# Kernel optimization log

Hardware: AMD Instinct MI355X
Metric: run time of the kernel (lower is better)

## Reference

```python
import jax, jax.numpy as jnp
import numpy as np

S = 4   # stride
NH = 4  # n_heads
NP = 4  # n_points


def conv2d(x, w, b, pad):
    out = jax.lax.conv_general_dilated(x, w, (1, 1), [(pad, pad), (pad, pad)],
                                       dimension_numbers=('NCHW', 'OIHW', 'NCHW'))
    return out + b[None, :, None, None]


def leaky(x):
    return jnp.where(x >= 0, x, 0.1 * x)


def seq_net(x, w0, b0, w1, b1, w2, b2, w3, b3):
    x = leaky(conv2d(x, w0, b0, 0))
    x = leaky(conv2d(x, w1, b1, 1))
    x = leaky(conv2d(x, w2, b2, 1))
    return conv2d(x, w3, b3, 0)


def fold_s(x, C, hs, ws):
    # inverse of unfold(kernel=S, stride=S): (N, C*S*S, hs*ws) -> (N, C, hs*S, ws*S)
    N = x.shape[0]
    x = x.reshape(N, C, S, S, hs, ws)
    return x.transpose(0, 1, 4, 2, 5, 3).reshape(N, C, hs * S, ws * S)


def unfold_s(x):
    # (N, C, h, w) -> (N, C*S*S, h//S, w//S), kernel=S, stride=S
    N, C, h, w = x.shape
    hs, ws = h // S, w // S
    x = x.reshape(N, C, hs, S, ws, S).transpose(0, 1, 3, 5, 2, 4)
    return x.reshape(N, C * S * S, hs, ws)


def avgpool_s(x):
    # adaptive_avg_pool2d (h,w)->(h/S,w/S) == mean over SxS blocks
    N, C, h, w = x.shape
    return x.reshape(N, C, h // S, S, w // S, S).mean(axis=(3, 5))


def grid_sample_nearest(img, grid):
    # img (N,C,H,W); grid (N,A,B,2) normalized; nearest, zeros padding, align_corners=True
    N, C, H, W = img.shape
    ix = jnp.round((grid[..., 0] + 1.0) * 0.5 * (W - 1))
    iy = jnp.round((grid[..., 1] + 1.0) * 0.5 * (H - 1))
    valid = (ix >= 0) & (ix <= W - 1) & (iy >= 0) & (iy <= H - 1)
    ixi = jnp.clip(ix, 0, W - 1).astype(jnp.int32)
    iyi = jnp.clip(iy, 0, H - 1).astype(jnp.int32)
    out = jax.vmap(lambda im, yy, xx: im[:, yy, xx])(img, iyi, ixi)  # (N,C,A,B)
    return out * valid[:, None].astype(img.dtype)


def ltff_forward(anchor_feat, sparse_feat_set_s1, flow_buffers,
                 so_w0, so_b0, so_w1, so_b1, so_w2, so_b2, so_w3, so_b3,
                 aw_w0, aw_b0, aw_w1, aw_b1, aw_w2, aw_b2, aw_w3, aw_b3,
                 fusion_w, fusion_b):
    n, c, h, w = anchor_feat.shape
    t = sparse_feat_set_s1.shape[1]
    hs, ws = h // S, w // S
    ch = c // NH  # per-head channels

    gy, gx = jnp.meshgrid(jnp.arange(hs), jnp.arange(ws), indexing='ij')
    loc_ref = jnp.stack([gx, gy], 0).astype(flow_buffers.dtype)[None, None]  # (1,1,2,hs,ws)
    location_feat = flow_buffers + loc_ref  # (n,t,2,hs,ws)

    # flow-warp the (strided) sparse feature set; align_corners=True norm uses dim-1
    gf = location_feat.transpose(0, 1, 3, 4, 2)  # (n,t,hs,ws,2)
    gfx = 2.0 * gf[..., 0] / max(ws - 1, 1) - 1.0
    gfy = 2.0 * gf[..., 1] / max(hs - 1, 1) - 1.0
    grid1 = jnp.stack([gfx, gfy], -1).reshape(n * t, hs, ws, 2)

    sp = sparse_feat_set_s1.reshape(n * t, c * S * S, hs, ws)
    warp = grid_sample_nearest(sp, grid1)
    out_res = fold_s(warp.reshape(n * t, c * S * S, hs * ws), c, hs, ws)  # (n*t,c,h,w)
    out_ori = fold_s(sp.reshape(n * t, c * S * S, hs * ws), c, hs, ws)

    extra = jnp.concatenate([avgpool_s(out_ori), avgpool_s(out_res),
                             flow_buffers.reshape(n * t, 2, hs, ws)], axis=1)  # (n*t,2c+2,hs,ws)

    offsets = seq_net(extra, so_w0, so_b0, so_w1, so_b1, so_w2, so_b2, so_w3, so_b3)
    offsets = offsets.reshape(n * t, NH * NP, 2, hs, ws)
    attn = seq_net(extra, aw_w0, aw_b0, aw_w1, aw_b1, aw_w2, aw_b2, aw_w3, aw_b3)
    attn = (attn.reshape(n, t, NH, NP, hs, ws)
                .transpose(0, 2, 4, 5, 1, 3)
                .reshape(n * NH, hs, ws, t * NP))
    attn = jax.nn.softmax(attn, axis=-1)

    og = location_feat.reshape(n * t, 1, 2, hs, ws) + offsets  # (n*t, NH*NP, 2, hs, ws)
    og = og.transpose(0, 1, 3, 4, 2)
    ogx = 2.0 * og[..., 0] / ws - 1.0  # original divides by dim (not dim-1) here
    ogy = 2.0 * og[..., 1] / hs - 1.0
    og = jnp.stack([ogx, ogy], -1).reshape(n, t, NH, NP, hs * ws, 2)
    og = og.transpose(0, 1, 2, 4, 3, 5).reshape(n * t * NH, hs * ws, NP, 2)

    vals = out_ori.reshape(n * t * NH, ch, h, w)
    vals = unfold_s(vals)  # (n*t*NH, ch*S*S, hs, ws)
    sampled = grid_sample_nearest(vals, og)  # (n*t*NH, ch*S*S, hs*ws, NP)
    sampled = (sampled.reshape(n, t, NH, ch * S * S, hs, ws, NP)
                      .transpose(0, 2, 3, 4, 5, 1, 6)
                      .reshape(n * NH, ch * S * S, hs, ws, t * NP))

    out = (sampled * attn[:, None]).sum(-1)  # (n*NH, ch*S*S, hs, ws)
    out = fold_s(out.reshape(n * NH, ch * S * S, hs * ws), ch, hs, ws).reshape(n, c, h, w)
    out = conv2d(out, fusion_w, fusion_b, 1) + anchor_feat
    return out


def setup_inputs():
    key = jax.random.key(0)
    ks = jax.random.split(key, 16)
    n, t, c, h, w = 2, 3, 128, 192, 192
    hs, ws = h // S, w // S
    cin = 2 * c + 2  # 258
    m = 64
    f32 = jnp.float32
    def rn(k, shape, scale=1.0):
        return jax.random.normal(k, shape, dtype=f32) * scale
    return {
        'curr_feat': rn(ks[0], (n, c, h, w)),
        'anchor_feat': rn(ks[1], (n, c, h, w)),
        'sparse_feat_set_s1': rn(ks[2], (n, t, c * S * S, hs, ws)),
        'flow_buffers': rn(ks[3], (n, t, 2, hs, ws)),
        'so_w0': rn(ks[4], (m, cin, 1, 1), 0.05), 'so_b0': jnp.zeros((m,), f32),
        'so_w1': rn(ks[5], (m, m, 3, 3), 0.05), 'so_b1': jnp.zeros((m,), f32),
        'so_w2': rn(ks[6], (m, m, 3, 3), 0.05), 'so_b2': jnp.zeros((m,), f32),
        'so_w3': rn(ks[7], (NH * NP * 2, m, 1, 1), 0.05), 'so_b3': jnp.zeros((NH * NP * 2,), f32),
        'aw_w0': rn(ks[8], (m, cin, 1, 1), 0.05), 'aw_b0': jnp.zeros((m,), f32),
        'aw_w1': rn(ks[9], (m, m, 3, 3), 0.05), 'aw_b1': jnp.zeros((m,), f32),
        'aw_w2': rn(ks[10], (m, m, 3, 3), 0.05), 'aw_b2': jnp.zeros((m,), f32),
        'aw_w3': rn(ks[11], (NH * NP, m, 1, 1), 0.05), 'aw_b3': jnp.zeros((NH * NP,), f32),
        'fusion_w': rn(ks[12], (c, c, 3, 3), 0.02), 'fusion_b': jnp.zeros((c,), f32),
    }


def reference(curr_feat, anchor_feat, sparse_feat_set_s1, flow_buffers,
              so_w0, so_b0, so_w1, so_b1, so_w2, so_b2, so_w3, so_b3,
              aw_w0, aw_b0, aw_w1, aw_b1, aw_w2, aw_b2, aw_w3, aw_b3,
              fusion_w, fusion_b):
    # curr_feat is accepted by the original forward but never used
    return ltff_forward(anchor_feat, sparse_feat_set_s1, flow_buffers,
                        so_w0, so_b0, so_w1, so_b1, so_w2, so_b2, so_w3, so_b3,
                        aw_w0, aw_b0, aw_w1, aw_b1, aw_w2, aw_b2, aw_w3, aw_b3,
                        fusion_w, fusion_b)
```

## Files before the change

kernel.cpp:

```cpp
#include <hip/hip_runtime.h>

typedef unsigned short u16;
typedef unsigned int u32;
typedef __attribute__((ext_vector_type(8))) short bf16x8;
typedef __attribute__((ext_vector_type(4))) float f32x4;

#define HS   48
#define WSB  48
#define NPIX 2304
#define CCH  128
#define NT   6
#define CIN  258
#define HH   192
#define WW   192

#define EXTRA_OFF  0ull
#define OUTIMG_OFF 0ull
#define XA_OFF     4718592ull
#define XB_OFF     6488064ull
#define OFFS_OFF   8257536ull
#define ARAW_OFF   8699904ull
#define WT_OFF     8921088ull
#define SPT_OFF    4718592ull
#define ATTNW_OFF  11796480ull
#define SIDX_OFF   12017664ull
#define WBF_OFF    12238848ull

static __device__ __forceinline__ float leaky_f(float v) { return v >= 0.f ? v : 0.1f * v; }
static __device__ __forceinline__ u16 f2bf(float f) {
    u32 u = __float_as_uint(f);
    u = (u + 0x7fffu + ((u >> 16) & 1u)) >> 16;
    return (u16)u;
}
static __device__ __forceinline__ float bf2f(u16 v) {
    u32 u = ((u32)v) << 16;
    return __uint_as_float(u);
}

__global__ __launch_bounds__(256) void k_wprep(const float* __restrict__ fw, u16* __restrict__ wbf) {
    int i = blockIdx.x * 256 + threadIdx.x;
    int j  = i & 7;
    int g  = (i >> 3) & 3;
    int oc = (i >> 5) & 127;
    int kcd = i >> 12;
    int d = kcd >> 2, kc = kcd & 3;
    int ic = kc * 32 + g * 8 + j;
    wbf[i] = f2bf(fw[((size_t)oc * 128 + ic) * 9 + d]);
}

__global__ __launch_bounds__(256) void k_wprep2(const float* __restrict__ so_w1, const float* __restrict__ aw_w1,
                                                const float* __restrict__ so_w2, const float* __restrict__ aw_w2,
                                                float* __restrict__ wT) {
    int i = blockIdx.x * 256 + threadIdx.x;
    int l   = i / 73728;
    int r1  = i % 73728;
    int net = r1 / 36864;
    int r   = r1 % 36864;
    int ic  = r / 576;
    int t2  = r % 576;
    int tap = t2 >> 6, oc = t2 & 63;
    const float* src = l ? (net ? aw_w2 : so_w2) : (net ? aw_w1 : so_w1);
    wT[i] = src[(size_t)oc * 576 + ic * 9 + tap];
}

__global__ __launch_bounds__(256) void k_avgpool(const float* __restrict__ sp,
                                                 float* __restrict__ extra) {
    int idx = blockIdx.x * 256 + threadIdx.x;
    if (idx >= NT * CCH * NPIX) return;
    int pix = idx % NPIX;
    int cc  = (idx / NPIX) % CCH;
    int nt  = idx / (NPIX * CCH);
    const float* p = sp + ((size_t)nt * 2048 + (size_t)cc * 16) * NPIX + pix;
    float s = 0.f;
#pragma unroll
    for (int k = 0; k < 16; k++) s += p[(size_t)k * NPIX];
    extra[((size_t)nt * CIN + cc) * NPIX + pix] = s * 0.0625f;
}

__global__ __launch_bounds__(256) void k_extra_rest(const float* __restrict__ flow,
                                                    float* __restrict__ extra) {
    int idx = blockIdx.x * 256 + threadIdx.x;
    if (idx >= NT * 130 * NPIX) return;
    int pix = idx % NPIX;
    int cc  = (idx / NPIX) % 130;
    int nt  = idx / (NPIX * 130);
    float fx = flow[((size_t)nt * 2 + 0) * NPIX + pix];
    float fy = flow[((size_t)nt * 2 + 1) * NPIX + pix];
    if (cc >= 128) {
        extra[((size_t)nt * CIN + 256 + (cc - 128)) * NPIX + pix] = (cc == 128) ? fx : fy;
        return;
    }
    int x = pix % WSB, y = pix / WSB;
    float locx = fx + (float)x;
    float locy = fy + (float)y;
    float gfx = 2.0f * locx / 47.0f - 1.0f;
    float gfy = 2.0f * locy / 47.0f - 1.0f;
    float rx = rintf(((gfx + 1.0f) * 0.5f) * 47.0f);
    float ry = rintf(((gfy + 1.0f) * 0.5f) * 47.0f);
    bool valid = (rx >= 0.f) && (rx <= 47.f) && (ry >= 0.f) && (ry <= 47.f);
    int sx = (int)fminf(fmaxf(rx, 0.f), 47.f);
    int sy = (int)fminf(fmaxf(ry, 0.f), 47.f);
    float v = valid ? extra[((size_t)nt * CIN + cc) * NPIX + sy * WSB + sx] : 0.f;
    extra[((size_t)nt * CIN + 128 + cc) * NPIX + pix] = v;
}

__global__ __launch_bounds__(256) void k_conv1x1_l0(const float* __restrict__ extra,
                                                    const float* __restrict__ w_so, const float* __restrict__ b_so,
                                                    const float* __restrict__ w_aw, const float* __restrict__ b_aw,
                                                    float* __restrict__ xa) {
    __shared__ float ws_[16 * CIN];
    int tile = blockIdx.x;
    int nt   = blockIdx.y;
    int z    = blockIdx.z;
    int net = z >> 2, ocg = z & 3;
    const float* wsel = net ? w_aw : w_so;
    const float* bsel = net ? b_aw : b_so;
    for (int i = threadIdx.x; i < 16 * CIN; i += 256)
        ws_[i] = wsel[(size_t)(ocg * 16) * CIN + i];
    __syncthreads();
    int pix = tile * 256 + threadIdx.x;
    float acc[16];
#pragma unroll
    for (int o = 0; o < 16; o++) acc[o] = bsel[ocg * 16 + o];
    const float* in = extra + (size_t)nt * CIN * NPIX + pix;
    for (int ci = 0; ci < CIN; ci++) {
        float v = in[(size_t)ci * NPIX];
#pragma unroll
        for (int o = 0; o < 16; o++) acc[o] = fmaf(ws_[o * CIN + ci], v, acc[o]);
    }
    float* op = xa + (((size_t)net * NT + nt) * 64 + ocg * 16) * NPIX + pix;
#pragma unroll
    for (int o = 0; o < 16; o++) op[(size_t)o * NPIX] = leaky_f(acc[o]);
}

__global__ __launch_bounds__(256) void k_conv3x3(const float* __restrict__ xin,
                                                 const float* __restrict__ wT,
                                                 const float* __restrict__ b_so, const float* __restrict__ b_aw,
                                                 float* __restrict__ xout) {
    __shared__ float At[16][6][24];
    __shared__ float Bt[16][9][64];
    int tid = threadIdx.x;
    int txq = tid & 3, tyq = (tid >> 2) & 3, ocg = tid >> 4;
    int st = blockIdx.x;
    int x0 = (st % 3) * 16, y0 = (st / 3) * 4;
    int nt = blockIdx.y, net = blockIdx.z;
    const float* in  = xin + ((size_t)net * NT + nt) * 64 * NPIX;
    const float* wTn = wT + (size_t)net * 36864;
    const float* bsel = net ? b_aw : b_so;

    float acc[4][4];
#pragma unroll
    for (int o = 0; o < 4; o++) {
        float bv = bsel[ocg * 4 + o];
#pragma unroll
        for (int p = 0; p < 4; p++) acc[o][p] = bv;
    }

    for (int c0 = 0; c0 < 64; c0 += 16) {
        __syncthreads();
        for (int i = tid; i < 1728; i += 256) {
            int ic = i / 108, r = i % 108;
            int ry = r / 18, rx = r % 18;
            int gy = y0 + ry - 1, gx = x0 + rx - 1;
            float v = 0.f;
            if (gy >= 0 && gy < HS && gx >= 0 && gx < WSB)
                v = in[(size_t)(c0 + ic) * NPIX + gy * WSB + gx];
            At[ic][ry][rx] = v;
        }
        {
            const float* src = wTn + (size_t)c0 * 576;
            float* dst = &Bt[0][0][0];
            for (int i = tid; i < 9216; i += 256) dst[i] = src[i];
        }
        __syncthreads();
#pragma unroll 2
        for (int ic = 0; ic < 16; ic++) {
#pragma unroll
            for (int dy = 0; dy < 3; dy++) {
                f32x4 a0 = *reinterpret_cast<const f32x4*>(&At[ic][tyq + dy][4 * txq]);
                f32x4 a1 = *reinterpret_cast<const f32x4*>(&At[ic][tyq + dy][4 * txq + 4]);
#pragma unroll
                for (int dx = 0; dx < 3; dx++) {
                    f32x4 bv = *reinterpret_cast<const f32x4*>(&Bt[ic][dy * 3 + dx][4 * ocg]);
#pragma unroll
                    for (int p = 0; p < 4; p++) {
                        float av = (dx + p < 4) ? a0[dx + p] : a1[dx + p - 4];
#pragma unroll
                        for (int o = 0; o < 4; o++)
                            acc[o][p] = fmaf(bv[o], av, acc[o][p]);
                    }
                }
            }
        }
    }

    int py = y0 + tyq, pxb = x0 + 4 * txq;
#pragma unroll
    for (int o = 0; o < 4; o++) {
        f32x4 res;
#pragma unroll
        for (int p = 0; p < 4; p++) res[p] = leaky_f(acc[o][p]);
        float* op = xout + (((size_t)net * NT + nt) * 64 + ocg * 4 + o) * NPIX + py * WSB + pxb;
        *reinterpret_cast<f32x4*>(op) = res;
    }
}

__global__ __launch_bounds__(256) void k_conv1x1_l3(const float* __restrict__ xin,
                                                    const float* __restrict__ w_so, const float* __restrict__ b_so,
                                                    const float* __restrict__ w_aw, const float* __restrict__ b_aw,
                                                    float* __restrict__ offs, float* __restrict__ araw) {
    int pix = blockIdx.x * 256 + threadIdx.x;
    int nt = blockIdx.y;
    int net = blockIdx.z;
    const float* in = xin + ((size_t)net * NT + nt) * 64 * NPIX + pix;
    if (net == 0) {
        float acc[32];
#pragma unroll
        for (int o = 0; o < 32; o++) acc[o] = b_so[o];
        for (int ci = 0; ci < 64; ci++) {
            float v = in[(size_t)ci * NPIX];
#pragma unroll
            for (int o = 0; o < 32; o++) acc[o] = fmaf(w_so[o * 64 + ci], v, acc[o]);
        }
#pragma unroll
        for (int o = 0; o < 32; o++) offs[((size_t)nt * 32 + o) * NPIX + pix] = acc[o];
    } else {
        float acc[16];
#pragma unroll
        for (int o = 0; o < 16; o++) acc[o] = b_aw[o];
        for (int ci = 0; ci < 64; ci++) {
            float v = in[(size_t)ci * NPIX];
#pragma unroll
            for (int o = 0; o < 16; o++) acc[o] = fmaf(w_aw[o * 64 + ci], v, acc[o]);
        }
#pragma unroll
        for (int o = 0; o < 16; o++) araw[((size_t)nt * 16 + o) * NPIX + pix] = acc[o];
    }
}

__global__ __launch_bounds__(256) void k_softmax_idx(const float* __restrict__ araw,
                                                     const float* __restrict__ offs,
                                                     const float* __restrict__ flow,
                                                     float* __restrict__ attnw, int* __restrict__ sidx) {
    int idx = blockIdx.x * 256 + threadIdx.x;
    if (idx >= 2 * 4 * NPIX) return;
    int pix  = idx % NPIX;
    int head = (idx / NPIX) & 3;
    int n    = idx / (NPIX * 4);
    int x = pix % WSB, y = pix / WSB;
    float a[12];
#pragma unroll
    for (int t = 0; t < 3; t++)
#pragma unroll
        for (int p = 0; p < 4; p++)
            a[t * 4 + p] = araw[(((size_t)(n * 3 + t)) * 16 + head * 4 + p) * NPIX + pix];
    float mx = a[0];
#pragma unroll
    for (int k = 1; k < 12; k++) mx = fmaxf(mx, a[k]);
    float ssum = 0.f;
#pragma unroll
    for (int k = 0; k < 12; k++) { a[k] = expf(a[k] - mx); ssum += a[k]; }
    float inv = 1.0f / ssum;
#pragma unroll
    for (int t = 0; t < 3; t++) {
        int nt = n * 3 + t;
        float fx = flow[((size_t)nt * 2 + 0) * NPIX + pix];
        float fy = flow[((size_t)nt * 2 + 1) * NPIX + pix];
        float locx = fx + (float)x;
        float locy = fy + (float)y;
#pragma unroll
        for (int p = 0; p < 4; p++) {
            int hp = head * 4 + p;
            float gx_ = locx + offs[(((size_t)nt) * 32 + hp * 2 + 0) * NPIX + pix];
            float gy_ = locy + offs[(((size_t)nt) * 32 + hp * 2 + 1) * NPIX + pix];
            float ngx = 2.0f * gx_ / 48.0f - 1.0f;
            float ngy = 2.0f * gy_ / 48.0f - 1.0f;
            float rx = rintf(((ngx + 1.0f) * 0.5f) * 47.0f);
            float ry = rintf(((ngy + 1.0f) * 0.5f) * 47.0f);
            bool valid = (rx >= 0.f) && (rx <= 47.f) && (ry >= 0.f) && (ry <= 47.f);
            int sx = (int)fminf(fmaxf(rx, 0.f), 47.f);
            int sy = (int)fminf(fmaxf(ry, 0.f), 47.f);
            int k = t * 4 + p;
            attnw[(size_t)idx * 12 + k] = valid ? a[k] * inv : 0.f;
            sidx[(size_t)idx * 12 + k]  = sy * WSB + sx;
        }
    }
}

__global__ __launch_bounds__(256) void k_transpose(const float* __restrict__ sp,
                                                   u16* __restrict__ spT, int n) {
    __shared__ float tile[64][65];
    int tid = threadIdx.x;
    int pix0 = blockIdx.x * 64;
    int ch0  = blockIdx.y * 64;
    int tl   = blockIdx.z;
    int nt = n * 3 + tl;
    const float* base = sp + ((size_t)nt * 2048 + ch0) * NPIX + pix0;
#pragma unroll
    for (int k = 0; k < 16; k++) {
        int row = k * 4 + (tid >> 6);
        int col = tid & 63;
        tile[row][col] = base[(size_t)row * NPIX + col];
    }
    __syncthreads();
#pragma unroll
    for (int k = 0; k < 2; k++) {
        int task = k * 256 + tid;
        int pl = task >> 3;
        int c0 = (task & 7) * 8;
        u16 pk[8];
#pragma unroll
        for (int j = 0; j < 8; j++) pk[j] = f2bf(tile[c0 + j][pl]);
        *reinterpret_cast<int4*>(spT + ((size_t)tl * NPIX + pix0 + pl) * 2048 + ch0 + c0) =
            *reinterpret_cast<const int4*>(pk);
    }
}

__global__ __launch_bounds__(256) void k_gather2(const u16* __restrict__ spT,
                                                 const float* __restrict__ attnw,
                                                 const int* __restrict__ sidx,
                                                 u16* __restrict__ outimg, int n) {
    __shared__ u16 sArr[2048 + 128];
    int tid = threadIdx.x;
    int pix = blockIdx.x;
    int y = pix / WSB, x = pix % WSB;
    int h = tid >> 6;
    int lane = tid & 63;
    size_t ab = ((size_t)(n * 4 + h) * NPIX + pix) * 12;
    float acc[8] = {};
#pragma unroll
    for (int t = 0; t < 3; t++) {
#pragma unroll
        for (int p = 0; p < 4; p++) {
            int k = t * 4 + p;
            float w = attnw[ab + k];
            int idx = sidx[ab + k];
            bf16x8 v = *reinterpret_cast<const bf16x8*>(
                spT + ((size_t)t * NPIX + idx) * 2048 + h * 512 + lane * 8);
#pragma unroll
            for (int j = 0; j < 8; j++)
                acc[j] = fmaf(w, bf2f((u16)v[j]), acc[j]);
        }
    }
    int c0 = h * 512 + lane * 8;
    int si = c0 + (c0 >> 4);
    u16 pk[8];
#pragma unroll
    for (int j = 0; j < 8; j++) pk[j] = f2bf(acc[j]);
    *reinterpret_cast<int4*>(&sArr[si]) = *reinterpret_cast<const int4*>(pk);
    __syncthreads();
    int opix = tid >> 4;
    int oc0 = (tid & 15) * 8;
    u16 ov[8];
#pragma unroll
    for (int j = 0; j < 8; j++) {
        int oc = oc0 + j;
        int ch = (oc >> 5) * 512 + (oc & 31) * 16 + opix;
        ov[j] = sArr[ch + (ch >> 4)];
    }
    int hq = y * 4 + (opix >> 2);
    int wq = x * 4 + (opix & 3);
    *reinterpret_cast<int4*>(outimg + (((size_t)(n * HH + hq) * WW + wq) << 7) + oc0) =
        *reinterpret_cast<const int4*>(ov);
}

__global__ __launch_bounds__(256, 3) void k_fusion_mfma(const u16* __restrict__ img,
                                                        const u16* __restrict__ wbf,
                                                        const float* __restrict__ bias,
                                                        const float* __restrict__ anchor,
                                                        float* __restrict__ out) {
    __shared__ __align__(16) u16 lds_in[180 * 128];

    const int tid = threadIdx.x;
    const int px0 = blockIdx.x * 16;
    const int py0 = blockIdx.y * 8;
    const int nb  = blockIdx.z >> 1;
    const int ocq = blockIdx.z & 1;
    const int lane = tid & 63;
    const int w = tid >> 6;
    const int r = lane & 15, g = lane >> 4;

    char* lin_b = reinterpret_cast<char*>(lds_in);

    for (int i = tid; i < 180 * 16; i += 256) {
        int p = i >> 4, c16 = i & 15;
        int hy = p / 18, hx = p % 18;
        int gy = py0 + hy - 1, gx = px0 + hx - 1;
        int4 v = make_int4(0, 0, 0, 0);
        if (gy >= 0 && gy < HH && gx >= 0 && gx < WW)
            v = *reinterpret_cast<const int4*>(img + (((size_t)(nb * HH + gy) * WW + gx) << 7) + (c16 << 3));
        *reinterpret_cast<int4*>(lin_b + p * 256 + (((c16 ^ (p & 7)) << 4))) = v;
    }

    const u16* wb = wbf + (size_t)(ocq * 64 + r) * 32 + g * 8;

    f32x4 acc[2][4] = {};
    bf16x8 b[2][4];
#pragma unroll
    for (int n = 0; n < 4; n++)
        b[0][n] = *reinterpret_cast<const bf16x8*>(wb + (size_t)n * 512);

    __syncthreads();

#pragma unroll
    for (int ph = 0; ph < 36; ph++) {
        const int d = ph >> 2, kc = ph & 3;
        const int dy = d / 3, dx = d % 3;
        if (ph < 35) {
#pragma unroll
            for (int n = 0; n < 4; n++)
                b[(ph + 1) & 1][n] = *reinterpret_cast<const bf16x8*>(
                    wb + (size_t)(ph + 1) * 4096 + (size_t)n * 512);
        }
        const int c16 = kc * 4 + g;
        bf16x8 a[2];
#pragma unroll
        for (int m = 0; m < 2; m++) {
            int hp = (2 * w + m + dy) * 18 + (r + dx);
            a[m] = *reinterpret_cast<const bf16x8*>(lin_b + hp * 256 + (((c16 ^ (hp & 7)) << 4)));
        }
#pragma unroll
        for (int m = 0; m < 2; m++)
#pragma unroll
            for (int n = 0; n < 4; n++)
                acc[m][n] = __builtin_amdgcn_mfma_f32_16x16x32_bf16(a[m], b[ph & 1][n], acc[m][n], 0, 0, 0);
    }

    float bs[4];
#pragma unroll
    for (int n = 0; n < 4; n++) bs[n] = bias[ocq * 64 + n * 16 + r];
#pragma unroll
    for (int m = 0; m < 2; m++) {
        int gy = py0 + 2 * w + m;
#pragma unroll
        for (int n = 0; n < 4; n++) {
            int oc = ocq * 64 + n * 16 + r;
            size_t oa = ((size_t)(nb * CCH + oc)) * (HH * WW) + (size_t)gy * WW + px0 + g * 4;
            f32x4 av = *reinterpret_cast<const f32x4*>(anchor + oa);
            f32x4 res;
#pragma unroll
            for (int q = 0; q < 4; q++) res[q] = acc[m][n][q] + bs[n] + av[q];
            *reinterpret_cast<f32x4*>(out + oa) = res;
        }
    }
}

extern "C" void kernel_launch(void* const* d_in, const int* in_sizes, int n_in,
                              void* d_out, int out_size, void* d_ws, size_t ws_size,
                              hipStream_t stream) {
    (void)in_sizes; (void)n_in; (void)out_size; (void)ws_size;
    const float* anchor = (const float*)d_in[1];
    const float* sp     = (const float*)d_in[2];
    const float* flow   = (const float*)d_in[3];
    const float* so_w0 = (const float*)d_in[4];  const float* so_b0 = (const float*)d_in[5];
    const float* so_w1 = (const float*)d_in[6];  const float* so_b1 = (const float*)d_in[7];
    const float* so_w2 = (const float*)d_in[8];  const float* so_b2 = (const float*)d_in[9];
    const float* so_w3 = (const float*)d_in[10]; const float* so_b3 = (const float*)d_in[11];
    const float* aw_w0 = (const float*)d_in[12]; const float* aw_b0 = (const float*)d_in[13];
    const float* aw_w1 = (const float*)d_in[14]; const float* aw_b1 = (const float*)d_in[15];
    const float* aw_w2 = (const float*)d_in[16]; const float* aw_b2 = (const float*)d_in[17];
    const float* aw_w3 = (const float*)d_in[18]; const float* aw_b3 = (const float*)d_in[19];
    const float* fw    = (const float*)d_in[20]; const float* fb    = (const float*)d_in[21];

    float* ws     = (float*)d_ws;
    float* extra  = ws + EXTRA_OFF;
    float* xa     = ws + XA_OFF;
    float* xb     = ws + XB_OFF;
    float* offs   = ws + OFFS_OFF;
    float* araw   = ws + ARAW_OFF;
    float* wT     = ws + WT_OFF;
    float* attnw  = ws + ATTNW_OFF;
    int*   sidx   = (int*)(ws + SIDX_OFF);
    u16*   wbf    = (u16*)(ws + WBF_OFF);
    u16*   spT    = (u16*)(ws + SPT_OFF);
    u16*   outimg = (u16*)(ws + OUTIMG_OFF);
    float* outp   = (float*)d_out;

    k_wprep<<<dim3(576), 256, 0, stream>>>(fw, wbf);
    k_wprep2<<<dim3(576), 256, 0, stream>>>(so_w1, aw_w1, so_w2, aw_w2, wT);
    k_avgpool<<<dim3((NT * CCH * NPIX + 255) / 256), 256, 0, stream>>>(sp, extra);
    k_extra_rest<<<dim3((NT * 130 * NPIX + 255) / 256), 256, 0, stream>>>(flow, extra);
    k_conv1x1_l0<<<dim3(9, 6, 8), 256, 0, stream>>>(extra, so_w0, so_b0, aw_w0, aw_b0, xa);
    k_conv3x3<<<dim3(36, 6, 2), 256, 0, stream>>>(xa, wT, so_b1, aw_b1, xb);
    k_conv3x3<<<dim3(36, 6, 2), 256, 0, stream>>>(xb, wT + 73728, so_b2, aw_b2, xa);
    k_conv1x1_l3<<<dim3(9, 6, 2), 256, 0, stream>>>(xa, so_w3, so_b3, aw_w3, aw_b3, offs, araw);
    k_softmax_idx<<<dim3((2 * 4 * NPIX + 255) / 256), 256, 0, stream>>>(araw, offs, flow, attnw, sidx);
    for (int n = 0; n < 2; n++) {
        k_transpose<<<dim3(36, 32, 3), 256, 0, stream>>>(sp, spT, n);
        k_gather2<<<dim3(NPIX), 256, 0, stream>>>(spT, attnw, sidx, outimg, n);
    }
    k_fusion_mfma<<<dim3(WW / 16, HH / 8, 4), 256, 0, stream>>>(outimg, wbf, fb, anchor, outp);
}
```

Baseline: 297.0 us.

## Fuse avgpool with bf16 transpose of sparse features into one pass

Adds a kernel that reads each 64x64 tile of the sparse feature set once, writes the bf16 pixel-major transpose for all frames, and computes the 4x4-channel average pooling from the same shared-memory tile. This replaces the separate avgpool pass and the per-batch transpose passes, so the large input is read once instead of twice. It needs a larger workspace layout, and the old path is kept as a fallback when the workspace is too small.

```diff
diff --git a/kernel.cpp b/kernel.cpp
--- a/kernel.cpp
+++ b/kernel.cpp
@@ -25,6 +25,19 @@
 #define ATTNW_OFF  11796480ull
 #define SIDX_OFF   12017664ull
 #define WBF_OFF    12238848ull
+
+#define SPT2_OFF    0ull
+#define EXTRA2_OFF  14155776ull
+#define OUTIMG2_OFF 14155776ull
+#define XA2_OFF     17722368ull
+#define XB2_OFF     19491840ull
+#define OFFS2_OFF   21261312ull
+#define ARAW2_OFF   21703680ull
+#define WT2_OFF     21924864ull
+#define ATTNW2_OFF  22072320ull
+#define SIDX2_OFF   22293504ull
+#define WBF2_OFF    22514688ull
+#define TOTAL2_F32  22588416ull
 
 static __device__ __forceinline__ float leaky_f(float v) { return v >= 0.f ? v : 0.1f * v; }
 static __device__ __forceinline__ u16 f2bf(float f) {
@@ -75,6 +88,44 @@
 #pragma unroll
     for (int k = 0; k < 16; k++) s += p[(size_t)k * NPIX];
     extra[((size_t)nt * CIN + cc) * NPIX + pix] = s * 0.0625f;
+}
+
+__global__ __launch_bounds__(256) void k_spprep(const float* __restrict__ sp,
+                                                u16* __restrict__ spT2,
+                                                float* __restrict__ extra) {
+    __shared__ float tile[64][65];
+    int tid = threadIdx.x;
+    int pix0 = blockIdx.x * 64;
+    int ch0  = blockIdx.y * 64;
+    int nt   = blockIdx.z;
+    const float* base = sp + ((size_t)nt * 2048 + ch0) * NPIX + pix0;
+#pragma unroll
+    for (int k = 0; k < 16; k++) {
+        int row = k * 4 + (tid >> 6);
+        int col = tid & 63;
+        tile[row][col] = base[(size_t)row * NPIX + col];
+    }
+    __syncthreads();
+#pragma unroll
+    for (int k = 0; k < 2; k++) {
+        int task = k * 256 + tid;
+        int pl = task >> 3;
+        int c0 = (task & 7) * 8;
+        u16 pk[8];
+#pragma unroll
+        for (int j = 0; j < 8; j++) pk[j] = f2bf(tile[c0 + j][pl]);
+        *reinterpret_cast<int4*>(spT2 + ((size_t)nt * NPIX + pix0 + pl) * 2048 + ch0 + c0) =
+            *reinterpret_cast<const int4*>(pk);
+    }
+    {
+        int ccl = tid >> 6;
+        int col = tid & 63;
+        float s = 0.f;
+#pragma unroll
+        for (int k = 0; k < 16; k++) s += tile[ccl * 16 + k][col];
+        int cc = (ch0 >> 4) + ccl;
+        extra[((size_t)nt * CIN + cc) * NPIX + pix0 + col] = s * 0.0625f;
+    }
 }
 
 __global__ __launch_bounds__(256) void k_extra_rest(const float* __restrict__ flow,
@@ -448,7 +499,7 @@
 extern "C" void kernel_launch(void* const* d_in, const int* in_sizes, int n_in,
                               void* d_out, int out_size, void* d_ws, size_t ws_size,
                               hipStream_t stream) {
-    (void)in_sizes; (void)n_in; (void)out_size; (void)ws_size;
+    (void)in_sizes; (void)n_in; (void)out_size;
     const float* anchor = (const float*)d_in[1];
     const float* sp     = (const float*)d_in[2];
     const float* flow   = (const float*)d_in[3];
@@ -462,32 +513,53 @@
     const float* aw_w3 = (const float*)d_in[18]; const float* aw_b3 = (const float*)d_in[19];
     const float* fw    = (const float*)d_in[20]; const float* fb    = (const float*)d_in[21];
 
-    float* ws     = (float*)d_ws;
-    float* extra  = ws + EXTRA_OFF;
-    float* xa     = ws + XA_OFF;
-    float* xb     = ws + XB_OFF;
-    float* offs   = ws + OFFS_OFF;
-    float* araw   = ws + ARAW_OFF;
-    float* wT     = ws + WT_OFF;
-    float* attnw  = ws + ATTNW_OFF;
-    int*   sidx   = (int*)(ws + SIDX_OFF);
-    u16*   wbf    = (u16*)(ws + WBF_OFF);
-    u16*   spT    = (u16*)(ws + SPT_OFF);
-    u16*   outimg = (u16*)(ws + OUTIMG_OFF);
-    float* outp   = (float*)d_out;
+    float* ws   = (float*)d_ws;
+    float* outp = (float*)d_out;
+    const bool big = ws_size >= TOTAL2_F32 * 4ull;
+
+    float* extra; float* xa; float* xb; float* offs; float* araw; float* wT;
+    float* attnw; int* sidx; u16* wbf; u16* outimg;
+
+    if (big) {
+        extra = ws + EXTRA2_OFF;  xa = ws + XA2_OFF;    xb = ws + XB2_OFF;
+        offs  = ws + OFFS2_OFF;   araw = ws + ARAW2_OFF; wT = ws + WT2_OFF;
+        attnw = ws + ATTNW2_OFF;  sidx = (int*)(ws + SIDX2_OFF);
+        wbf   = (u16*)(ws + WBF2_OFF);  outimg = (u16*)(ws + OUTIMG2_OFF);
+    } else {
+        extra = ws + EXTRA_OFF;   xa = ws + XA_OFF;     xb = ws + XB_OFF;
+        offs  = ws + OFFS_OFF;    araw = ws + ARAW_OFF;  wT = ws + WT_OFF;
+        attnw = ws + ATTNW_OFF;   sidx = (int*)(ws + SIDX_OFF);
+        wbf   = (u16*)(ws + WBF_OFF);   outimg = (u16*)(ws + OUTIMG_OFF);
+    }
 
     k_wprep<<<dim3(576), 256, 0, stream>>>(fw, wbf);
     k_wprep2<<<dim3(576), 256, 0, stream>>>(so_w1, aw_w1, so_w2, aw_w2, wT);
-    k_avgpool<<<dim3((NT * CCH * NPIX + 255) / 256), 256, 0, stream>>>(sp, extra);
-    k_extra_rest<<<dim3((NT * 130 * NPIX + 255) / 256), 256, 0, stream>>>(flow, extra);
-    k_conv1x1_l0<<<dim3(9, 6, 8), 256, 0, stream>>>(extra, so_w0, so_b0, aw_w0, aw_b0, xa);
-    k_conv3x3<<<dim3(36, 6, 2), 256, 0, stream>>>(xa, wT, so_b1, aw_b1, xb);
-    k_conv3x3<<<dim3(36, 6, 2), 256, 0, stream>>>(xb, wT + 73728, so_b2, aw_b2, xa);
-    k_conv1x1_l3<<<dim3(9, 6, 2), 256, 0, stream>>>(xa, so_w3, so_b3, aw_w3, aw_b3, offs, araw);
-    k_softmax_idx<<<dim3((2 * 4 * NPIX + 255) / 256), 256, 0, stream>>>(araw, offs, flow, attnw, sidx);
-    for (int n = 0; n < 2; n++) {
-        k_transpose<<<dim3(36, 32, 3), 256, 0, stream>>>(sp, spT, n);
-        k_gather2<<<dim3(NPIX), 256, 0, stream>>>(spT, attnw, sidx, outimg, n);
+
+    if (big) {
+        u16* spT2 = (u16*)(ws + SPT2_OFF);
+        k_spprep<<<dim3(36, 32, 6), 256, 0, stream>>>(sp, spT2, extra);
+        k_extra_rest<<<dim3((NT * 130 * NPIX + 255) / 256), 256, 0, stream>>>(flow, extra);
+        k_conv1x1_l0<<<dim3(9, 6, 8), 256, 0, stream>>>(extra, so_w0, so_b0, aw_w0, aw_b0, xa);
+        k_conv3x3<<<dim3(36, 6, 2), 256, 0, stream>>>(xa, wT, so_b1, aw_b1, xb);
+        k_conv3x3<<<dim3(36, 6, 2), 256, 0, stream>>>(xb, wT + 73728, so_b2, aw_b2, xa);
+        k_conv1x1_l3<<<dim3(9, 6, 2), 256, 0, stream>>>(xa, so_w3, so_b3, aw_w3, aw_b3, offs, araw);
+        k_softmax_idx<<<dim3((2 * 4 * NPIX + 255) / 256), 256, 0, stream>>>(araw, offs, flow, attnw, sidx);
+        for (int n = 0; n < 2; n++)
+            k_gather2<<<dim3(NPIX), 256, 0, stream>>>(spT2 + (size_t)n * 3 * NPIX * 2048,
+                                                      attnw, sidx, outimg, n);
+    } else {
+        u16* spT = (u16*)(ws + SPT_OFF);
+        k_avgpool<<<dim3((NT * CCH * NPIX + 255) / 256), 256, 0, stream>>>(sp, extra);
+        k_extra_rest<<<dim3((NT * 130 * NPIX + 255) / 256), 256, 0, stream>>>(flow, extra);
+        k_conv1x1_l0<<<dim3(9, 6, 8), 256, 0, stream>>>(extra, so_w0, so_b0, aw_w0, aw_b0, xa);
+        k_conv3x3<<<dim3(36, 6, 2), 256, 0, stream>>>(xa, wT, so_b1, aw_b1, xb);
+        k_conv3x3<<<dim3(36, 6, 2), 256, 0, stream>>>(xb, wT + 73728, so_b2, aw_b2, xa);
+        k_conv1x1_l3<<<dim3(9, 6, 2), 256, 0, stream>>>(xa, so_w3, so_b3, aw_w3, aw_b3, offs, araw);
+        k_softmax_idx<<<dim3((2 * 4 * NPIX + 255) / 256), 256, 0, stream>>>(araw, offs, flow, attnw, sidx);
+        for (int n = 0; n < 2; n++) {
+            k_transpose<<<dim3(36, 32, 3), 256, 0, stream>>>(sp, spT, n);
+            k_gather2<<<dim3(NPIX), 256, 0, stream>>>(spT, attnw, sidx, outimg, n);
+        }
     }
     k_fusion_mfma<<<dim3(WW / 16, HH / 8, 4), 256, 0, stream>>>(outimg, wbf, fb, anchor, outp);
 }
```

New measurement: 281.4 us (median of 2 runs). 5.3% less time.
